# Performance work log

Measured on AMD Instinct MI355X. Metric: run time of the kernel, lower is better.

The kernel has to match this reference:

```python
import jax, jax.numpy as jnp
import numpy as np

D_IN = 2048   # input obs dim
D_H = 2048    # hidden / expert dim
D_V = 2048    # attention value dim
D_A = 256     # attention key/query dim
N_EXP = 16    # expert_nums
N_TASK = 10   # task_nums
D_T = 2048    # tower hidden dim
D_OUT = 512   # output_shape


def setup_inputs() -> dict:
    key = jax.random.key(0)
    ks = jax.random.split(key, 18)
    s = lambda k, shape: (jax.random.normal(k, shape, dtype=jnp.float32) * 0.02)
    z = lambda shape: jnp.zeros(shape, dtype=jnp.float32)
    return {
        "x": jax.random.normal(ks[0], (D_IN,), dtype=jnp.float32),
        # base: 2-layer MLP d_in -> d_h -> d_h
        "W1": s(ks[1], (D_IN, D_H)), "b1": z((D_H,)),
        "W2": s(ks[2], (D_H, D_H)), "b2": z((D_H,)),
        # per-expert MLP (stacked over expert axis)
        "W_exp": s(ks[3], (N_EXP, D_H, D_H)), "b_exp": z((N_EXP, D_H)),
        # per-expert attention value / key heads
        "W_v": s(ks[4], (N_EXP, D_H, D_V)), "b_v": z((N_EXP, D_V)),
        "W_k": s(ks[5], (N_EXP, D_H, D_A)), "b_k": z((N_EXP, D_A)),
        # per-task query heads: Linear(task_nums -> d_att)
        "W_q": s(ks[6], (N_TASK, N_TASK, D_A)), "b_q": z((N_TASK, D_A)),
        # tower + last
        "W_t": s(ks[7], (D_V, D_T)), "b_t": z((D_T,)),
        "W_l": s(ks[8], (D_T, D_OUT)), "b_l": z((D_OUT,)),
        "task_id": 3,
    }


def reference(x, W1, b1, W2, b2, W_exp, b_exp, W_v, b_v, W_k, b_k,
              W_q, b_q, W_t, b_t, W_l, b_l, task_id):
    relu = jax.nn.relu
    # one-hot task index, as in the torch forward
    task_idx = jax.nn.one_hot(task_id, N_TASK, dtype=x.dtype)
    # base MLP
    out = relu(x @ W1 + b1)            # [d_h]
    out = relu(out @ W2 + b2)          # [d_h]
    # all experts batched (collapses the python loop over experts)
    e = relu(jnp.einsum('h,nhk->nk', out, W_exp) + b_exp)   # [n, d_h]
    v = jnp.einsum('nh,nhv->nv', e, W_v) + b_v              # [n, d_v]
    k = jnp.einsum('nh,nha->na', e, W_k) + b_k              # [n, d_a]
    # task-specific query
    q = task_idx @ W_q[task_id] + b_q[task_id]              # [d_a]
    expkq = k @ q                                           # [n]
    # NOTE: original sums v_i * expkq_i (raw scores, NOT the normalized alphas)
    res = expkq @ v                                         # [d_v]
    out = relu(res @ W_t + b_t)                             # [d_t]
    return out @ W_l + b_l                                  # [d_out]
```

## Files before the change

### kernel.cpp

```cpp
#include <hip/hip_runtime.h>

#define THREADS 256

template<int TCOLS>
__global__ __launch_bounds__(THREADS) void matvec_k(
    const float* __restrict__ x, const float* __restrict__ W,
    float* __restrict__ P,
    int K, int slice_h, int nslices,
    long x_stride, long w_stride)
{
    const int n = blockIdx.z;
    const float* xn = x + (long)n * x_stride;
    const float* Wn = W + (long)n * w_stride;
    float* Pn = P + ((long)n * nslices + blockIdx.y) * K;

    const int h0 = blockIdx.y * slice_h;
    constexpr int TPR = TCOLS / 4;
    constexpr int RPI = THREADS / TPR;
    const int tid = threadIdx.x;
    const int lane_r = tid % TPR;
    const int row_off = tid / TPR;
    const int c = blockIdx.x * TCOLS + 4 * lane_r;

    extern __shared__ char smem[];
    float* xs = (float*)smem;
    int*   idx = (int*)(smem + (size_t)slice_h * 4);
    __shared__ int cnt;

    if (tid == 0) cnt = 0;
    __syncthreads();
    for (int i = tid; i < slice_h; i += THREADS) {
        float v = xn[h0 + i];
        xs[i] = v;
        if (v != 0.0f) { int p = atomicAdd(&cnt, 1); idx[p] = i; }
    }
    __syncthreads();
    const int m = cnt;

    float ax = 0.f, ay = 0.f, az = 0.f, aw = 0.f;
    for (int j = row_off; j < m; j += RPI) {
        const int i = idx[j];
        const float4 w4 = *(const float4*)(Wn + (long)(h0 + i) * K + c);
        const float xv = xs[i];
        ax = fmaf(xv, w4.x, ax);
        ay = fmaf(xv, w4.y, ay);
        az = fmaf(xv, w4.z, az);
        aw = fmaf(xv, w4.w, aw);
    }

    if constexpr (RPI > 1) {
        __shared__ float red[THREADS * 4];
        red[tid * 4 + 0] = ax; red[tid * 4 + 1] = ay;
        red[tid * 4 + 2] = az; red[tid * 4 + 3] = aw;
        __syncthreads();
        if (row_off == 0) {
            #pragma unroll
            for (int g = 1; g < RPI; g++) {
                const int o = (tid + g * TPR) * 4;
                ax += red[o + 0]; ay += red[o + 1];
                az += red[o + 2]; aw += red[o + 3];
            }
            float4 r; r.x = ax; r.y = ay; r.z = az; r.w = aw;
            *(float4*)(Pn + c) = r;
        }
    } else {
        float4 r; r.x = ax; r.y = ay; r.z = az; r.w = aw;
        *(float4*)(Pn + c) = r;
    }
}

template<bool RELU, bool HAS_BIAS>
__global__ __launch_bounds__(THREADS) void reduce_k(
    const float* __restrict__ P, const float* __restrict__ b,
    float* __restrict__ y, int K, int nslices)
{
    const int n = blockIdx.y;
    const int col = blockIdx.x * 64 + (threadIdx.x & 63);
    const int grp = threadIdx.x >> 6;
    const float* Pn = P + (long)n * nslices * K + col;
    float s = 0.f;
    for (int i = grp; i < nslices; i += 4) s += Pn[(long)i * K];
    __shared__ float red[4][64];
    red[grp][threadIdx.x & 63] = s;
    __syncthreads();
    if (threadIdx.x < 64) {
        float t = red[0][threadIdx.x] + red[1][threadIdx.x] +
                  red[2][threadIdx.x] + red[3][threadIdx.x];
        if (HAS_BIAS) t += b[(long)n * K + col];
        if (RELU) t = fmaxf(t, 0.f);
        y[(long)n * K + col] = t;
    }
}

__global__ __launch_bounds__(THREADS) void qprep_k(
    const float* __restrict__ Wq, const float* __restrict__ bq,
    const float* __restrict__ bk, const int* __restrict__ task,
    float* __restrict__ q, float* __restrict__ bkq)
{
    const int tid = threadIdx.x;
    const int t = task[0];
    __shared__ float qs[256];
    float qv = Wq[((long)t * 10 + t) * 256 + tid] + bq[(long)t * 256 + tid];
    qs[tid] = qv; q[tid] = qv;
    __syncthreads();
    const int wave = tid >> 6, lane = tid & 63;
    for (int n = wave; n < 16; n += 4) {
        float s = 0.f;
        for (int a = lane; a < 256; a += 64) s += bk[n * 256 + a] * qs[a];
        for (int o = 32; o; o >>= 1) s += __shfl_down(s, o, 64);
        if (lane == 0) bkq[n] = s;
    }
}

__global__ __launch_bounds__(THREADS) void kq_mv_k(
    const float* __restrict__ eact, const float* __restrict__ Wk,
    const float* __restrict__ q, float* __restrict__ pkq)
{
    const int n = blockIdx.y, s = blockIdx.x;
    const int h0 = s * 256;
    const int tid = threadIdx.x;
    __shared__ float xs[256], qs[256];
    __shared__ int idx[256];
    __shared__ int cnt;
    __shared__ float wred[4];
    if (tid == 0) cnt = 0;
    qs[tid] = q[tid];
    __syncthreads();
    float v = eact[n * 2048 + h0 + tid];
    xs[tid] = v;
    if (v != 0.0f) { int p = atomicAdd(&cnt, 1); idx[p] = tid; }
    __syncthreads();
    const int m = cnt;
    const int lane_r = tid & 63, row_off = tid >> 6;
    const float q0 = qs[4 * lane_r], q1 = qs[4 * lane_r + 1];
    const float q2 = qs[4 * lane_r + 2], q3 = qs[4 * lane_r + 3];
    float acc = 0.f;
    for (int j = row_off; j < m; j += 4) {
        const int i = idx[j];
        const float4 w4 = *(const float4*)(Wk + ((long)n * 2048 + h0 + i) * 256 + 4 * lane_r);
        acc += xs[i] * (w4.x * q0 + w4.y * q1 + w4.z * q2 + w4.w * q3);
    }
    for (int o = 32; o; o >>= 1) acc += __shfl_down(acc, o, 64);
    if ((tid & 63) == 0) wred[tid >> 6] = acc;
    __syncthreads();
    if (tid == 0) pkq[n * 8 + s] = wred[0] + wred[1] + wred[2] + wred[3];
}

__global__ __launch_bounds__(THREADS) void weight_k(
    const float* __restrict__ eact, const float* __restrict__ pkq,
    const float* __restrict__ bkq, const float* __restrict__ bv,
    float* __restrict__ wbuf, float* __restrict__ resb)
{
    __shared__ float ekqs[16];
    const int tid = threadIdx.x;
    if (tid < 16) {
        float s = bkq[tid];
        #pragma unroll
        for (int j = 0; j < 8; j++) s += pkq[tid * 8 + j];
        ekqs[tid] = s;
    }
    __syncthreads();
    const int b = blockIdx.x;
    if (b < 128) {
        const int g = b * 256 + tid;
        wbuf[g] = ekqs[g >> 11] * eact[g];
    } else {
        const int j = (b - 128) * 256 + tid;
        float s = 0.f;
        #pragma unroll
        for (int n = 0; n < 16; n++) s += ekqs[n] * bv[n * 2048 + j];
        resb[j] = s;
    }
}

extern "C" void kernel_launch(void* const* d_in, const int* in_sizes, int n_in,
                              void* d_out, int out_size, void* d_ws, size_t ws_size,
                              hipStream_t stream)
{
    const float* x    = (const float*)d_in[0];
    const float* W1   = (const float*)d_in[1];
    const float* b1   = (const float*)d_in[2];
    const float* W2   = (const float*)d_in[3];
    const float* b2   = (const float*)d_in[4];
    const float* Wexp = (const float*)d_in[5];
    const float* bexp = (const float*)d_in[6];
    const float* Wv   = (const float*)d_in[7];
    const float* bv   = (const float*)d_in[8];
    const float* Wk   = (const float*)d_in[9];
    const float* bk   = (const float*)d_in[10];
    const float* Wq   = (const float*)d_in[11];
    const float* bq   = (const float*)d_in[12];
    const float* Wt   = (const float*)d_in[13];
    const float* bt   = (const float*)d_in[14];
    const float* Wl   = (const float*)d_in[15];
    const float* bl   = (const float*)d_in[16];
    const int*   task = (const int*)d_in[17];

    float* ws   = (float*)d_ws;
    float* P1   = ws;
    float* y1   = ws + 262144;
    float* P2   = ws + 264192;
    float* y2   = ws + 526336;
    float* Pexp = ws + 528384;
    float* eact = ws + 1576960;
    float* q    = ws + 1609728;
    float* bkq  = ws + 1609984;
    float* pkq  = ws + 1610000;
    float* wbuf = ws + 1610128;
    float* resb = ws + 1642896;
    float* Pv   = ws + 1644944;
    float* resp = ws + 2169232;
    float* Pt   = ws + 2171280;
    float* tact = ws + 2433424;
    float* Pl   = ws + 2435472;

    qprep_k<<<1, 256, 0, stream>>>(Wq, bq, bk, task, q, bkq);

    matvec_k<1024><<<dim3(2, 128, 1), THREADS, 16 * 8, stream>>>(
        x, W1, P1, 2048, 16, 128, 0, 0);
    reduce_k<true, true><<<dim3(32, 1), THREADS, 0, stream>>>(P1, b1, y1, 2048, 128);

    matvec_k<1024><<<dim3(2, 128, 1), THREADS, 16 * 8, stream>>>(
        y1, W2, P2, 2048, 16, 128, 0, 0);
    reduce_k<true, true><<<dim3(32, 1), THREADS, 0, stream>>>(P2, b2, y2, 2048, 128);

    matvec_k<1024><<<dim3(2, 32, 16), THREADS, 64 * 8, stream>>>(
        y2, Wexp, Pexp, 2048, 64, 32, 0, 2048L * 2048);
    reduce_k<true, true><<<dim3(32, 16), THREADS, 0, stream>>>(Pexp, bexp, eact, 2048, 32);

    kq_mv_k<<<dim3(8, 16), THREADS, 0, stream>>>(eact, Wk, q, pkq);

    weight_k<<<136, THREADS, 0, stream>>>(eact, pkq, bkq, bv, wbuf, resb);

    matvec_k<1024><<<dim3(2, 256, 1), THREADS, 128 * 8, stream>>>(
        wbuf, Wv, Pv, 2048, 128, 256, 0, 0);
    reduce_k<false, true><<<dim3(32, 1), THREADS, 0, stream>>>(Pv, resb, resp, 2048, 256);

    matvec_k<1024><<<dim3(2, 128, 1), THREADS, 16 * 8, stream>>>(
        resp, Wt, Pt, 2048, 16, 128, 0, 0);
    reduce_k<true, true><<<dim3(32, 1), THREADS, 0, stream>>>(Pt, bt, tact, 2048, 128);

    matvec_k<512><<<dim3(1, 64, 1), THREADS, 32 * 8, stream>>>(
        tact, Wl, Pl, 512, 32, 64, 0, 0);
    reduce_k<false, true><<<dim3(8, 1), THREADS, 0, stream>>>(Pl, bl, (float*)d_out, 512, 64);
}
```

Baseline: 677.0 us.

## Fuse split-K reductions into consumer matvec kernels and drop weight prep kernel

Each matvec now reduces the previous stage's split-K partials, adds bias and applies ReLU on its own input slice, so the separate reduce_k launches disappear. The Wv stage now computes per-expert values and the expkq weighting is folded into the tower matvec's input reduction, which also removes weight_k. This cuts kernel launches and intermediate round trips through memory. In exchange, each block redundantly re-reads many partial-sum rows.

```diff
diff --git a/kernel.cpp b/kernel.cpp
--- a/kernel.cpp
+++ b/kernel.cpp
@@ -42,12 +42,9 @@
         const int i = idx[j];
         const float4 w4 = *(const float4*)(Wn + (long)(h0 + i) * K + c);
         const float xv = xs[i];
-        ax = fmaf(xv, w4.x, ax);
-        ay = fmaf(xv, w4.y, ay);
-        az = fmaf(xv, w4.z, az);
-        aw = fmaf(xv, w4.w, aw);
-    }
-
+        ax = fmaf(xv, w4.x, ax); ay = fmaf(xv, w4.y, ay);
+        az = fmaf(xv, w4.z, az); aw = fmaf(xv, w4.w, aw);
+    }
     if constexpr (RPI > 1) {
         __shared__ float red[THREADS * 4];
         red[tid * 4 + 0] = ax; red[tid * 4 + 1] = ay;
@@ -69,6 +66,134 @@
     }
 }
 
+template<int TCOLS, int SH, bool RELU>
+__global__ __launch_bounds__(THREADS) void matvec_rx(
+    const float* __restrict__ Pprev, const float* __restrict__ bias,
+    const float* __restrict__ W, float* __restrict__ Pout,
+    int K, int nsl_prev, int prev_K, int nsl_out,
+    long pprev_stride, long bias_stride, long w_stride)
+{
+    const int n = blockIdx.z;
+    const int h0 = blockIdx.y * SH;
+    const float* Pp = Pprev + (long)n * pprev_stride;
+    const float* bn = bias + (long)n * bias_stride;
+    const float* Wn = W + (long)n * w_stride;
+    float* Pn = Pout + ((long)n * nsl_out + blockIdx.y) * K;
+
+    constexpr int G = THREADS / SH;
+    const int tid = threadIdx.x;
+    __shared__ float part[THREADS];
+    __shared__ float xs[SH];
+    __shared__ int idx[SH];
+    __shared__ int cnt;
+
+    {
+        const int i = tid % SH, g = tid / SH;
+        float a = 0.f;
+        for (int sp = g; sp < nsl_prev; sp += G)
+            a += Pp[(long)sp * prev_K + h0 + i];
+        part[g * SH + i] = a;
+    }
+    if (tid == 0) cnt = 0;
+    __syncthreads();
+    if (tid < SH) {
+        float v = part[tid];
+        #pragma unroll
+        for (int g = 1; g < G; g++) v += part[g * SH + tid];
+        v += bn[h0 + tid];
+        if (RELU) v = fmaxf(v, 0.f);
+        xs[tid] = v;
+        if (v != 0.0f) { int p = atomicAdd(&cnt, 1); idx[p] = tid; }
+    }
+    __syncthreads();
+    const int m = cnt;
+
+    constexpr int TPR = TCOLS / 4;
+    constexpr int RPI = THREADS / TPR;
+    const int lane_r = tid % TPR;
+    const int row_off = tid / TPR;
+    const int c = blockIdx.x * TCOLS + 4 * lane_r;
+
+    float ax = 0.f, ay = 0.f, az = 0.f, aw = 0.f;
+    for (int j = row_off; j < m; j += RPI) {
+        const int i = idx[j];
+        const float4 w4 = *(const float4*)(Wn + (long)(h0 + i) * K + c);
+        const float xv = xs[i];
+        ax = fmaf(xv, w4.x, ax); ay = fmaf(xv, w4.y, ay);
+        az = fmaf(xv, w4.z, az); aw = fmaf(xv, w4.w, aw);
+    }
+    if constexpr (RPI > 1) {
+        __shared__ float red[THREADS * 4];
+        red[tid * 4 + 0] = ax; red[tid * 4 + 1] = ay;
+        red[tid * 4 + 2] = az; red[tid * 4 + 3] = aw;
+        __syncthreads();
+        if (row_off == 0) {
+            #pragma unroll
+            for (int g = 1; g < RPI; g++) {
+                const int o = (tid + g * TPR) * 4;
+                ax += red[o + 0]; ay += red[o + 1];
+                az += red[o + 2]; aw += red[o + 3];
+            }
+            float4 r; r.x = ax; r.y = ay; r.z = az; r.w = aw;
+            *(float4*)(Pn + c) = r;
+        }
+    } else {
+        float4 r; r.x = ax; r.y = ay; r.z = az; r.w = aw;
+        *(float4*)(Pn + c) = r;
+    }
+}
+
+template<int TCOLS>
+__global__ __launch_bounds__(THREADS) void matvec_tx(
+    const float* __restrict__ Pv, const float* __restrict__ bv,
+    const float* __restrict__ pkq, const float* __restrict__ bkq,
+    const float* __restrict__ Wt, float* __restrict__ Pout,
+    int K, int nsl_out)
+{
+    const int h0 = blockIdx.y * 16;
+    const int tid = threadIdx.x;
+    __shared__ float ekqs[16];
+    __shared__ float part[THREADS];
+    __shared__ float xs[16];
+
+    if (tid < 16) {
+        float e = bkq[tid];
+        #pragma unroll
+        for (int j = 0; j < 8; j++) e += pkq[tid * 8 + j];
+        ekqs[tid] = e;
+    }
+    __syncthreads();
+    {
+        const int i = tid % 16, n = tid / 16;
+        const float* Pp = Pv + (long)n * 16 * 2048;
+        float a = 0.f;
+        #pragma unroll
+        for (int sp = 0; sp < 16; sp++) a += Pp[(long)sp * 2048 + h0 + i];
+        a += bv[(long)n * 2048 + h0 + i];
+        part[tid] = ekqs[n] * a;
+    }
+    __syncthreads();
+    if (tid < 16) {
+        float v = 0.f;
+        #pragma unroll
+        for (int g = 0; g < 16; g++) v += part[g * 16 + tid];
+        xs[tid] = v;
+    }
+    __syncthreads();
+
+    const int c = blockIdx.x * TCOLS + 4 * tid;
+    float ax = 0.f, ay = 0.f, az = 0.f, aw = 0.f;
+    #pragma unroll 4
+    for (int i = 0; i < 16; i++) {
+        const float4 w4 = *(const float4*)(Wt + (long)(h0 + i) * K + c);
+        const float xv = xs[i];
+        ax = fmaf(xv, w4.x, ax); ay = fmaf(xv, w4.y, ay);
+        az = fmaf(xv, w4.z, az); aw = fmaf(xv, w4.w, aw);
+    }
+    float4 r; r.x = ax; r.y = ay; r.z = az; r.w = aw;
+    *(float4*)(Pout + (long)blockIdx.y * K + c) = r;
+}
+
 template<bool RELU, bool HAS_BIAS>
 __global__ __launch_bounds__(THREADS) void reduce_k(
     const float* __restrict__ P, const float* __restrict__ b,
@@ -112,9 +237,10 @@
     }
 }
 
-__global__ __launch_bounds__(THREADS) void kq_mv_k(
-    const float* __restrict__ eact, const float* __restrict__ Wk,
-    const float* __restrict__ q, float* __restrict__ pkq)
+__global__ __launch_bounds__(THREADS) void kq2_k(
+    const float* __restrict__ Pexp, const float* __restrict__ bexp,
+    const float* __restrict__ Wk, const float* __restrict__ q,
+    float* __restrict__ pkq)
 {
     const int n = blockIdx.y, s = blockIdx.x;
     const int h0 = s * 256;
@@ -125,10 +251,15 @@
     __shared__ float wred[4];
     if (tid == 0) cnt = 0;
     qs[tid] = q[tid];
-    __syncthreads();
-    float v = eact[n * 2048 + h0 + tid];
-    xs[tid] = v;
-    if (v != 0.0f) { int p = atomicAdd(&cnt, 1); idx[p] = tid; }
+    const float* Pp = Pexp + (long)n * 32 * 2048;
+    float a = 0.f;
+    #pragma unroll 8
+    for (int sp = 0; sp < 32; sp++) a += Pp[(long)sp * 2048 + h0 + tid];
+    a += bexp[(long)n * 2048 + h0 + tid];
+    a = fmaxf(a, 0.f);
+    __syncthreads();
+    xs[tid] = a;
+    if (a != 0.0f) { int p = atomicAdd(&cnt, 1); idx[p] = tid; }
     __syncthreads();
     const int m = cnt;
     const int lane_r = tid & 63, row_off = tid >> 6;
@@ -144,33 +275,6 @@
     if ((tid & 63) == 0) wred[tid >> 6] = acc;
     __syncthreads();
     if (tid == 0) pkq[n * 8 + s] = wred[0] + wred[1] + wred[2] + wred[3];
-}
-
-__global__ __launch_bounds__(THREADS) void weight_k(
-    const float* __restrict__ eact, const float* __restrict__ pkq,
-    const float* __restrict__ bkq, const float* __restrict__ bv,
-    float* __restrict__ wbuf, float* __restrict__ resb)
-{
-    __shared__ float ekqs[16];
-    const int tid = threadIdx.x;
-    if (tid < 16) {
-        float s = bkq[tid];
-        #pragma unroll
-        for (int j = 0; j < 8; j++) s += pkq[tid * 8 + j];
-        ekqs[tid] = s;
-    }
-    __syncthreads();
-    const int b = blockIdx.x;
-    if (b < 128) {
-        const int g = b * 256 + tid;
-        wbuf[g] = ekqs[g >> 11] * eact[g];
-    } else {
-        const int j = (b - 128) * 256 + tid;
-        float s = 0.f;
-        #pragma unroll
-        for (int n = 0; n < 16; n++) s += ekqs[n] * bv[n * 2048 + j];
-        resb[j] = s;
-    }
 }
 
 extern "C" void kernel_launch(void* const* d_in, const int* in_sizes, int n_in,
@@ -198,49 +302,38 @@
 
     float* ws   = (float*)d_ws;
     float* P1   = ws;
-    float* y1   = ws + 262144;
-    float* P2   = ws + 264192;
-    float* y2   = ws + 526336;
-    float* Pexp = ws + 528384;
-    float* eact = ws + 1576960;
-    float* q    = ws + 1609728;
-    float* bkq  = ws + 1609984;
-    float* pkq  = ws + 1610000;
-    float* wbuf = ws + 1610128;
-    float* resb = ws + 1642896;
-    float* Pv   = ws + 1644944;
-    float* resp = ws + 2169232;
-    float* Pt   = ws + 2171280;
-    float* tact = ws + 2433424;
-    float* Pl   = ws + 2435472;
+    float* P2   = ws + 262144;
+    float* Pexp = ws + 524288;
+    float* Pv   = ws + 1572864;
+    float* Pt   = ws + 2097152;
+    float* Pl   = ws + 2359296;
+    float* q    = ws + 2392064;
+    float* bkq  = ws + 2392320;
+    float* pkq  = ws + 2392336;
 
     qprep_k<<<1, 256, 0, stream>>>(Wq, bq, bk, task, q, bkq);
 
     matvec_k<1024><<<dim3(2, 128, 1), THREADS, 16 * 8, stream>>>(
         x, W1, P1, 2048, 16, 128, 0, 0);
-    reduce_k<true, true><<<dim3(32, 1), THREADS, 0, stream>>>(P1, b1, y1, 2048, 128);
-
-    matvec_k<1024><<<dim3(2, 128, 1), THREADS, 16 * 8, stream>>>(
-        y1, W2, P2, 2048, 16, 128, 0, 0);
-    reduce_k<true, true><<<dim3(32, 1), THREADS, 0, stream>>>(P2, b2, y2, 2048, 128);
-
-    matvec_k<1024><<<dim3(2, 32, 16), THREADS, 64 * 8, stream>>>(
-        y2, Wexp, Pexp, 2048, 64, 32, 0, 2048L * 2048);
-    reduce_k<true, true><<<dim3(32, 16), THREADS, 0, stream>>>(Pexp, bexp, eact, 2048, 32);
-
-    kq_mv_k<<<dim3(8, 16), THREADS, 0, stream>>>(eact, Wk, q, pkq);
-
-    weight_k<<<136, THREADS, 0, stream>>>(eact, pkq, bkq, bv, wbuf, resb);
-
-    matvec_k<1024><<<dim3(2, 256, 1), THREADS, 128 * 8, stream>>>(
-        wbuf, Wv, Pv, 2048, 128, 256, 0, 0);
-    reduce_k<false, true><<<dim3(32, 1), THREADS, 0, stream>>>(Pv, resb, resp, 2048, 256);
-
-    matvec_k<1024><<<dim3(2, 128, 1), THREADS, 16 * 8, stream>>>(
-        resp, Wt, Pt, 2048, 16, 128, 0, 0);
-    reduce_k<true, true><<<dim3(32, 1), THREADS, 0, stream>>>(Pt, bt, tact, 2048, 128);
-
-    matvec_k<512><<<dim3(1, 64, 1), THREADS, 32 * 8, stream>>>(
-        tact, Wl, Pl, 512, 32, 64, 0, 0);
-    reduce_k<false, true><<<dim3(8, 1), THREADS, 0, stream>>>(Pl, bl, (float*)d_out, 512, 64);
-}
+
+    matvec_rx<1024, 16, true><<<dim3(2, 128, 1), THREADS, 0, stream>>>(
+        P1, b1, W2, P2, 2048, 128, 2048, 128, 0, 0, 0);
+
+    matvec_rx<1024, 64, true><<<dim3(2, 32, 16), THREADS, 0, stream>>>(
+        P2, b2, Wexp, Pexp, 2048, 128, 2048, 32, 0, 0, 2048L * 2048);
+
+    kq2_k<<<dim3(8, 16), THREADS, 0, stream>>>(Pexp, bexp, Wk, q, pkq);
+
+    matvec_rx<1024, 128, true><<<dim3(2, 16, 16), THREADS, 0, stream>>>(
+        Pexp, bexp, Wv, Pv, 2048, 32, 2048, 16,
+        32L * 2048, 2048, 2048L * 2048);
+
+    matvec_tx<1024><<<dim3(2, 128, 1), THREADS, 0, stream>>>(
+        Pv, bv, pkq, bkq, Wt, Pt, 2048, 128);
+
+    matvec_rx<512, 32, true><<<dim3(1, 64, 1), THREADS, 0, stream>>>(
+        Pt, bt, Wl, Pl, 512, 128, 2048, 64, 0, 0, 0);
+
+    reduce_k<false, true><<<dim3(8, 1), THREADS, 0, stream>>>(
+        Pl, bl, (float*)d_out, 512, 64);
+}
```

Result: faster. 633.0 us (-6.5%).
